# Kernel tuning notes

Measured on AMD Instinct MI355X. Metric: run time of the kernel, lower is better.

## Reference

```python
import jax, jax.numpy as jnp
import numpy as np

L, B, D_IN, H, N, NUM_LAYERS = 2048, 16, 64, 512, 64, 4


def setup_inputs() -> dict:
    key = jax.random.key(0)
    ks = jax.random.split(key, 9)
    x = jax.random.normal(ks[0], (L, B, D_IN), dtype=jnp.float32)
    enc_W = jax.random.normal(ks[1], (D_IN, H), dtype=jnp.float32) / np.sqrt(D_IN)
    enc_b = jax.random.normal(ks[2], (H,), dtype=jnp.float32) * 0.01
    # Per-layer S4D parameters, stacked along leading layer axis.
    log_dt = jax.random.uniform(ks[3], (NUM_LAYERS, H), dtype=jnp.float32,
                                minval=np.log(1e-3), maxval=np.log(1e-1))
    log_A_re = jnp.log(0.5 * jnp.ones((NUM_LAYERS, H, N), dtype=jnp.float32))
    A_im = jnp.broadcast_to(np.pi * jnp.arange(N, dtype=jnp.float32),
                            (NUM_LAYERS, H, N)).copy()
    C_re = jax.random.normal(ks[4], (NUM_LAYERS, H, N), dtype=jnp.float32)
    C_im = jax.random.normal(ks[5], (NUM_LAYERS, H, N), dtype=jnp.float32)
    Dskip = jax.random.normal(ks[6], (NUM_LAYERS, H), dtype=jnp.float32)
    return {"x": x, "enc_W": enc_W, "enc_b": enc_b, "log_dt": log_dt,
            "log_A_re": log_A_re, "A_im": A_im, "C_re": C_re, "C_im": C_im,
            "Dskip": Dskip}


def _s4d_layer(u, log_dt, log_A_re, A_im, C_re, C_im, Dskip):
    """u: [L,B,H] real. Diagonal SSM recurrent scan (ZOH discretization)."""
    dt = jnp.exp(log_dt)[:, None]                      # [H,1]
    A = -jnp.exp(log_A_re) + 1j * A_im                 # [H,N] complex, Re<0
    dA = jnp.exp(dt * A)                               # [H,N]
    dB = (dA - 1.0) / A                                # [H,N]
    C = (C_re + 1j * C_im).astype(jnp.complex64)       # [H,N]

    def step(s, u_t):                                  # s:[B,H,N] c64, u_t:[B,H]
        s = dA * s + dB * u_t[..., None]
        y = 2.0 * jnp.einsum('hn,bhn->bh', C, s).real + Dskip * u_t
        return s, y.astype(u_t.dtype)

    s0 = jnp.zeros((u.shape[1], u.shape[2], A.shape[-1]), dtype=jnp.complex64)
    sT, ys = jax.lax.scan(step, s0, u)
    return ys, sT


def reference(x, enc_W, enc_b, log_dt, log_A_re, A_im, C_re, C_im, Dskip):
    # batch_first=False: x is [L,B,D_IN]; torch code transposes to [B,L,·],
    # applies encoder, runs layers, transposes back -> equivalent to keeping
    # time-major [L,B,H] throughout.
    h = x @ enc_W + enc_b                              # [L,B,H]
    states_re, states_im = [], []
    for i in range(NUM_LAYERS):
        h, sT = _s4d_layer(h, log_dt[i], log_A_re[i], A_im[i],
                           C_re[i], C_im[i], Dskip[i])
        states_re.append(sT.real)
        states_im.append(sT.imag)
    return h, jnp.stack(states_re), jnp.stack(states_im)
```

## Files before the change

kernel.cpp:

```cpp
#include <hip/hip_runtime.h>
#include <math.h>

#define L_SEQ 2048
#define B_SZ 16
#define DIN 64
#define H_SZ 512
#define N_ST 64
#define N_LAYERS 4
#define Q_CHUNK 64
#define N_CHUNKS (L_SEQ / Q_CHUNK)
#define GSZ 4
#define N_GROUPS (N_CHUNKS / GSZ)
#define UPAD 2056
#define NTHR 768

typedef _Float16 f16;
typedef _Float16 f16x8 __attribute__((ext_vector_type(8)));
typedef _Float16 f16x4 __attribute__((ext_vector_type(4)));
typedef float    f32x4 __attribute__((ext_vector_type(4)));

struct cx { float r, i; };
__device__ __forceinline__ cx cmul(cx a, cx b) {
    return { a.r * b.r - a.i * b.i, a.r * b.i + a.i * b.r };
}

__device__ __forceinline__ void barrier_lgkm() {
    asm volatile("s_waitcnt lgkmcnt(0)\n\ts_barrier" ::: "memory");
}

__global__ __launch_bounds__(256, 4)
void encoder_mfma_kernel(const float* __restrict__ x, const float* __restrict__ W,
                         const float* __restrict__ bias, f16* __restrict__ out)
{
    __shared__ f16   x_sh[64][72];
    __shared__ f16   w_t[64][72];
    __shared__ float out_sh[64][68];
    __shared__ float b_sh[64];
    const int tid = threadIdx.x;
    const int bid = blockIdx.x;
    const int bb  = bid & 15;
    const int lt  = (bid >> 4) & 31;
    const int ht  = bid >> 9;
    const int l0 = lt * 64, h0 = ht * 64;

#pragma unroll
    for (int i = 0; i < 16; ++i) {
        int idx = tid + i * 256;
        int r = idx >> 6, c = idx & 63;
        x_sh[r][c] = (f16)x[((size_t)(l0 + r) * B_SZ + bb) * DIN + c];
        w_t[c][r]  = (f16)W[(size_t)r * H_SZ + h0 + c];
    }
    if (tid < 64) b_sh[tid] = bias[h0 + tid];
    __syncthreads();

    const int wave = tid >> 6;
    const int lane = tid & 63;
    const int frow = lane & 15;
    const int fk   = (lane >> 4) * 8;
    const int m0   = wave * 16;

    f16x8 a0 = *(const f16x8*)&w_t[m0 + frow][fk];
    f16x8 a1 = *(const f16x8*)&w_t[m0 + frow][fk + 32];
    float bv[4];
#pragma unroll
    for (int j = 0; j < 4; ++j) bv[j] = b_sh[m0 + (lane >> 4) * 4 + j];

#pragma unroll
    for (int nt = 0; nt < 4; ++nt) {
        f16x8 b0 = *(const f16x8*)&x_sh[nt * 16 + frow][fk];
        f16x8 b1 = *(const f16x8*)&x_sh[nt * 16 + frow][fk + 32];
        f32x4 acc = {0.f, 0.f, 0.f, 0.f};
        acc = __builtin_amdgcn_mfma_f32_16x16x32_f16(a0, b0, acc, 0, 0, 0);
        acc = __builtin_amdgcn_mfma_f32_16x16x32_f16(a1, b1, acc, 0, 0, 0);
#pragma unroll
        for (int j = 0; j < 4; ++j)
            out_sh[m0 + (lane >> 4) * 4 + j][nt * 16 + frow] = acc[j] + bv[j];
    }
    __syncthreads();

#pragma unroll
    for (int i = 0; i < 4; ++i) {
        int row = (tid >> 4) + i * 16;
        int c4  = (tid & 15) * 4;
        f32x4 v = *(const f32x4*)&out_sh[row][c4];
        f16x4 o;
#pragma unroll
        for (int k = 0; k < 4; ++k) o[k] = (f16)v[k];
        *(f16x4*)&out[((size_t)(h0 + row) * B_SZ + bb) * L_SEQ + l0 + c4] = o;
    }
}

__global__ __launch_bounds__(NTHR, 3)
void s4d_fused_kernel(f16* __restrict__ u_io,
                      const float* __restrict__ log_dt, const float* __restrict__ log_A_re,
                      const float* __restrict__ A_im, const float* __restrict__ C_re,
                      const float* __restrict__ C_im, const float* __restrict__ Dskip,
                      float* __restrict__ st_re, float* __restrict__ st_im)
{
    __shared__ f16   A_lds[192][72];
    __shared__ f16   G_lds[65][136];
    __shared__ f16   U_all[16][UPAD];
    __shared__ f16   S_buf[2][GSZ][16][136];
    __shared__ float dBv_sh[128];
    __shared__ float K_sh[64];
    __shared__ float w_sh[64][2];

    const int tid  = threadIdx.x;
    const int wave = tid >> 6;
    const int lane = tid & 63;
    const int h    = blockIdx.x;
    const int frow = lane & 15;
    const int fq   = lane >> 4;
    const int fk   = fq * 8;

    {
        const f16* ub = u_io + (size_t)h * B_SZ * L_SEQ;
        for (int u0 = tid; u0 < 16 * 256; u0 += NTHR) {
            int b = u0 >> 8, cidx = (u0 & 255) * 8;
            *(f16x8*)&U_all[b][cidx] = *(const f16x8*)&ub[(size_t)b * L_SEQ + cidx];
        }
    }
    f16* yb = u_io + (size_t)h * B_SZ * L_SEQ;

    for (int layer = 0; layer < N_LAYERS; ++layer) {
        const int ph = layer * H_SZ + h;
        const int pn = ph * N_ST + lane;

        {
            float dt   = expf(log_dt[ph]);
            float Are  = -expf(log_A_re[pn]);
            float Aim  = A_im[pn];
            float mg   = expf(dt * Are);
            float phs  = dt * Aim;
            cx dA1 = { mg * cosf(phs), mg * sinf(phs) };
            float invd = 1.0f / (Are * Are + Aim * Aim);
            float nr   = dA1.r - 1.0f;
            float dBr  = (nr * Are + dA1.i * Aim) * invd;
            float dBi  = (dA1.i * Are - nr * Aim) * invd;
            float Cr   = C_re[pn];
            float Ci   = C_im[pn];
            if (wave == 0) { dBv_sh[2 * lane] = dBr; dBv_sh[2 * lane + 1] = dBi; }

            const int role = wave & 3;
            const int seg  = wave >> 2;
            cx dA2  = cmul(dA1, dA1);
            cx dA4  = cmul(dA2, dA2);
            cx dA8  = cmul(dA4, dA4);
            cx dA16 = cmul(dA8, dA8);
            cx P = { 1.f, 0.f };
            int j0 = 0, jend = 21;
            if (seg >= 1) { P = cmul(cmul(dA16, dA4), dA1); j0 = 21; jend = 42; }
            if (seg == 2) { P = cmul(P, P); j0 = 42; jend = (role >= 2) ? 65 : 64; }
            for (int j = j0; j < jend; ++j) {
                if (role == 0)      A_lds[64  + lane][63 - j] = (f16)(P.r * dBr - P.i * dBi);
                else if (role == 1) A_lds[128 + lane][63 - j] = (f16)(P.r * dBi + P.i * dBr);
                else if (role == 2) G_lds[j][2 * lane]     = (f16)( 2.f * (Cr * P.r - Ci * P.i));
                else {
                    G_lds[j][2 * lane + 1] = (f16)(-2.f * (Cr * P.i + Ci * P.r));
                    if (j == 64) { w_sh[lane][0] = P.r; w_sh[lane][1] = P.i; }
                }
                P = cmul(P, dA1);
            }
        }
        barrier_lgkm();

        if (tid < 512) {
            const int t  = tid >> 3;
            const int l8 = tid & 7;
            f16x8 g0 = *(const f16x8*)&G_lds[t][l8 * 16];
            f16x8 g1 = *(const f16x8*)&G_lds[t][l8 * 16 + 8];
            f32x4 d0 = *(const f32x4*)&dBv_sh[l8 * 16];
            f32x4 d1 = *(const f32x4*)&dBv_sh[l8 * 16 + 4];
            f32x4 d2 = *(const f32x4*)&dBv_sh[l8 * 16 + 8];
            f32x4 d3 = *(const f32x4*)&dBv_sh[l8 * 16 + 12];
            float acc = 0.f;
#pragma unroll
            for (int k = 0; k < 4; ++k) {
                acc += (float)g0[k]     * d0[k];
                acc += (float)g0[k + 4] * d1[k];
                acc += (float)g1[k]     * d2[k];
                acc += (float)g1[k + 4] * d3[k];
            }
            acc += __shfl_xor(acc, 1);
            acc += __shfl_xor(acc, 2);
            acc += __shfl_xor(acc, 4);
            if (l8 == 0) K_sh[t] = acc;
        }
        barrier_lgkm();
        for (int e = tid; e < 64 * 64; e += NTHR) {
            int i = e >> 6, jc = e & 63;
            A_lds[i][jc] = (jc <= i) ? (f16)K_sh[i - jc] : (f16)0.f;
        }
        barrier_lgkm();

        const float Dv = Dskip[ph];
        f16x8 aRe0, aRe1, aIm0, aIm1;
        f16x8 aT0[2], aT1[2], aG[2][4];
        float wr4[4], wi4[4];
        float s_r[4] = {0.f,0.f,0.f,0.f}, s_i[4] = {0.f,0.f,0.f,0.f};
        if (wave < 4) {
            const int m0 = 16 * wave;
            aRe0 = *(const f16x8*)&A_lds[64  + m0 + frow][fk];
            aRe1 = *(const f16x8*)&A_lds[64  + m0 + frow][fk + 32];
            aIm0 = *(const f16x8*)&A_lds[128 + m0 + frow][fk];
            aIm1 = *(const f16x8*)&A_lds[128 + m0 + frow][fk + 32];
#pragma unroll
            for (int p = 0; p < 4; ++p) {
                int n = m0 + fq * 4 + p;
                wr4[p] = w_sh[n][0]; wi4[p] = w_sh[n][1];
            }
        } else {
            const int mh = (wave - 4) & 1;
#pragma unroll
            for (int mt = 0; mt < 2; ++mt) {
                const int r0 = 32 * mh + 16 * mt + frow;
                aT0[mt] = *(const f16x8*)&A_lds[r0][fk];
                aT1[mt] = *(const f16x8*)&A_lds[r0][fk + 32];
#pragma unroll
                for (int k4 = 0; k4 < 4; ++k4)
                    aG[mt][k4] = *(const f16x8*)&G_lds[1 + r0][fk + 32 * k4];
            }
        }
        f16x4 yh[2];

        for (int g = 0; g <= N_GROUPS + 1; ++g) {
            if (wave < 4) {
                if (g < N_GROUPS) {
                    const int gb = g & 1;
#pragma unroll
                    for (int j = 0; j < GSZ; ++j) {
                        f16x8 sf;
                        sf[0] = (f16)s_r[0]; sf[1] = (f16)s_i[0];
                        sf[2] = (f16)s_r[1]; sf[3] = (f16)s_i[1];
                        sf[4] = (f16)s_r[2]; sf[5] = (f16)s_i[2];
                        sf[6] = (f16)s_r[3]; sf[7] = (f16)s_i[3];
                        *(f16x8*)&S_buf[gb][j][frow][32 * wave + 8 * fq] = sf;
                        const int co = (g * GSZ + j) * 64;
                        f16x8 b0 = *(const f16x8*)&U_all[frow][co + fk];
                        f16x8 b1 = *(const f16x8*)&U_all[frow][co + fk + 32];
                        f32x4 aR = {0.f,0.f,0.f,0.f}, aI = {0.f,0.f,0.f,0.f};
                        aR = __builtin_amdgcn_mfma_f32_16x16x32_f16(aRe0, b0, aR, 0, 0, 0);
                        aR = __builtin_amdgcn_mfma_f32_16x16x32_f16(aRe1, b1, aR, 0, 0, 0);
                        aI = __builtin_amdgcn_mfma_f32_16x16x32_f16(aIm0, b0, aI, 0, 0, 0);
                        aI = __builtin_amdgcn_mfma_f32_16x16x32_f16(aIm1, b1, aI, 0, 0, 0);
#pragma unroll
                        for (int p = 0; p < 4; ++p) {
                            float nr2 = wr4[p] * s_r[p] - wi4[p] * s_i[p] + aR[p];
                            float ni2 = wi4[p] * s_r[p] + wr4[p] * s_i[p] + aI[p];
                            s_r[p] = nr2; s_i[p] = ni2;
                        }
                    }
                }
            } else {
                const int ow = wave - 4, jc = ow >> 1, mh = ow & 1;
                if (layer < N_LAYERS - 1 && g >= 2) {
                    const int co2 = ((g - 2) * GSZ + jc) * 64;
                    *(f16x4*)&U_all[frow][co2 + 32 * mh + fq * 4]      = yh[0];
                    *(f16x4*)&U_all[frow][co2 + 32 * mh + 16 + fq * 4] = yh[1];
                }
                if (g >= 1 && g <= N_GROUPS) {
                    const int gp = g - 1, pb = gp & 1;
                    const int co = (gp * GSZ + jc) * 64;
                    f16x8 b0 = *(const f16x8*)&U_all[frow][co + fk];
                    f16x8 b1 = *(const f16x8*)&U_all[frow][co + fk + 32];
                    f16x8 sv0 = *(const f16x8*)&S_buf[pb][jc][frow][fk];
                    f16x8 sv1 = *(const f16x8*)&S_buf[pb][jc][frow][fk + 32];
                    f16x8 sv2 = *(const f16x8*)&S_buf[pb][jc][frow][fk + 64];
                    f16x8 sv3 = *(const f16x8*)&S_buf[pb][jc][frow][fk + 96];
#pragma unroll
                    for (int mt = 0; mt < 2; ++mt) {
                        f32x4 acc = {0.f,0.f,0.f,0.f};
                        acc = __builtin_amdgcn_mfma_f32_16x16x32_f16(aT0[mt], b0, acc, 0, 0, 0);
                        acc = __builtin_amdgcn_mfma_f32_16x16x32_f16(aT1[mt], b1, acc, 0, 0, 0);
                        acc = __builtin_amdgcn_mfma_f32_16x16x32_f16(aG[mt][0], sv0, acc, 0, 0, 0);
                        acc = __builtin_amdgcn_mfma_f32_16x16x32_f16(aG[mt][1], sv1, acc, 0, 0, 0);
                        acc = __builtin_amdgcn_mfma_f32_16x16x32_f16(aG[mt][2], sv2, acc, 0, 0, 0);
                        acc = __builtin_amdgcn_mfma_f32_16x16x32_f16(aG[mt][3], sv3, acc, 0, 0, 0);
                        const int t0 = 32 * mh + 16 * mt + fq * 4;
                        f16x4 uf = *(const f16x4*)&U_all[frow][co + t0];
                        f16x4 o;
#pragma unroll
                        for (int k = 0; k < 4; ++k) o[k] = (f16)(acc[k] + Dv * (float)uf[k]);
                        if (layer == N_LAYERS - 1)
                            *(f16x4*)&yb[(size_t)frow * L_SEQ + co + t0] = o;
                        else
                            yh[mt] = o;
                    }
                }
            }
            barrier_lgkm();
        }

        if (wave < 4) {
#pragma unroll
            for (int p = 0; p < 4; ++p) {
                int n = 16 * wave + 4 * fq + p;
                size_t base = (((size_t)layer * B_SZ + frow) * H_SZ + h) * N_ST + n;
                st_re[base] = s_r[p];
                st_im[base] = s_i[p];
            }
        }
        __syncthreads();
    }
}

__global__ __launch_bounds__(256, 4)
void hbl_to_lbh_kernel(const f16* __restrict__ in, float* __restrict__ out)
{
    __shared__ float t_sh[64][65];
    const int tid = threadIdx.x, bid = blockIdx.x;
    const int bb = bid & 15, lt = (bid >> 4) & 31, ht = bid >> 9;
    const int l0 = lt * 64, h0 = ht * 64;
#pragma unroll
    for (int i = 0; i < 4; ++i) {
        int idx = tid + i * 256;
        int hh = idx >> 4, l4 = (idx & 15) * 4;
        f16x4 v = *(const f16x4*)&in[((size_t)(h0 + hh) * B_SZ + bb) * L_SEQ + l0 + l4];
#pragma unroll
        for (int k = 0; k < 4; ++k) t_sh[hh][l4 + k] = (float)v[k];
    }
    __syncthreads();
#pragma unroll
    for (int i = 0; i < 16; ++i) {
        int idx = tid + i * 256;
        int ll = idx >> 6, hh = idx & 63;
        out[((size_t)(l0 + ll) * B_SZ + bb) * H_SZ + h0 + hh] = t_sh[hh][ll];
    }
}

extern "C" void kernel_launch(void* const* d_in, const int* in_sizes, int n_in,
                              void* d_out, int out_size, void* d_ws, size_t ws_size,
                              hipStream_t stream)
{
    const float* x        = (const float*)d_in[0];
    const float* enc_W    = (const float*)d_in[1];
    const float* enc_b    = (const float*)d_in[2];
    const float* log_dt   = (const float*)d_in[3];
    const float* log_A_re = (const float*)d_in[4];
    const float* A_im     = (const float*)d_in[5];
    const float* C_re     = (const float*)d_in[6];
    const float* C_im     = (const float*)d_in[7];
    const float* Dskip    = (const float*)d_in[8];

    float* out_lbh = (float*)d_out;
    float* st_re   = out_lbh + (size_t)L_SEQ * B_SZ * H_SZ;
    float* st_im   = st_re + (size_t)N_LAYERS * B_SZ * H_SZ * N_ST;
    f16*   B0      = (f16*)d_ws;

    encoder_mfma_kernel<<<4096, 256, 0, stream>>>(x, enc_W, enc_b, B0);

    s4d_fused_kernel<<<512, NTHR, 0, stream>>>(B0, log_dt, log_A_re, A_im,
                                               C_re, C_im, Dskip, st_re, st_im);

    hbl_to_lbh_kernel<<<4096, 256, 0, stream>>>(B0, out_lbh);
}
```

Baseline: 243.3 us.

## Overlap next-layer SSM kernel setup with scan, swizzle LDS, rebalance output waves

Waves 8-11, formerly output waves, now build the next layer's A/G/K matrices during groups 1-3 of the current layer's scan. The per-layer setup with its barriers is taken off the critical path for layers 1-3. The output work is consolidated onto waves 4-7, each handling four M-tiles. U_all and S_buf padding is replaced by an XOR swizzle, and the transpose kernel now writes float4. The risk is a race: the next layer's setup overwrites A_lds/G_lds/w_sh while the current layer's waves hold register copies, which is only safe if every wave has loaded its fragments before g==1.

```diff
diff --git a/kernel.cpp b/kernel.cpp
--- a/kernel.cpp
+++ b/kernel.cpp
@@ -11,8 +11,9 @@
 #define N_CHUNKS (L_SEQ / Q_CHUNK)
 #define GSZ 4
 #define N_GROUPS (N_CHUNKS / GSZ)
-#define UPAD 2056
 #define NTHR 768
+
+#define USWZ(b, colf16) ((((colf16) * 2)) ^ (((b) & 7) << 4))
 
 typedef _Float16 f16;
 typedef _Float16 f16x8 __attribute__((ext_vector_type(8)));
@@ -99,8 +100,8 @@
 {
     __shared__ f16   A_lds[192][72];
     __shared__ f16   G_lds[65][136];
-    __shared__ f16   U_all[16][UPAD];
-    __shared__ f16   S_buf[2][GSZ][16][136];
+    __shared__ f16   U_all[16][2048];
+    __shared__ f16   S_buf[2][GSZ][16][128];
     __shared__ float dBv_sh[128];
     __shared__ float K_sh[64];
     __shared__ float w_sh[64][2];
@@ -116,8 +117,9 @@
     {
         const f16* ub = u_io + (size_t)h * B_SZ * L_SEQ;
         for (int u0 = tid; u0 < 16 * 256; u0 += NTHR) {
-            int b = u0 >> 8, cidx = (u0 & 255) * 8;
-            *(f16x8*)&U_all[b][cidx] = *(const f16x8*)&ub[(size_t)b * L_SEQ + cidx];
+            int b = u0 >> 8, c8 = (u0 & 255) * 8;
+            f16x8 v = *(const f16x8*)&ub[(size_t)b * L_SEQ + c8];
+            *(f16x8*)((char*)U_all[b] + USWZ(b, c8)) = v;
         }
     }
     f16* yb = u_io + (size_t)h * B_SZ * L_SEQ;
@@ -126,76 +128,77 @@
         const int ph = layer * H_SZ + h;
         const int pn = ph * N_ST + lane;
 
-        {
-            float dt   = expf(log_dt[ph]);
-            float Are  = -expf(log_A_re[pn]);
-            float Aim  = A_im[pn];
-            float mg   = expf(dt * Are);
-            float phs  = dt * Aim;
-            cx dA1 = { mg * cosf(phs), mg * sinf(phs) };
-            float invd = 1.0f / (Are * Are + Aim * Aim);
-            float nr   = dA1.r - 1.0f;
-            float dBr  = (nr * Are + dA1.i * Aim) * invd;
-            float dBi  = (dA1.i * Are - nr * Aim) * invd;
-            float Cr   = C_re[pn];
-            float Ci   = C_im[pn];
-            if (wave == 0) { dBv_sh[2 * lane] = dBr; dBv_sh[2 * lane + 1] = dBi; }
-
-            const int role = wave & 3;
-            const int seg  = wave >> 2;
-            cx dA2  = cmul(dA1, dA1);
-            cx dA4  = cmul(dA2, dA2);
-            cx dA8  = cmul(dA4, dA4);
-            cx dA16 = cmul(dA8, dA8);
-            cx P = { 1.f, 0.f };
-            int j0 = 0, jend = 21;
-            if (seg >= 1) { P = cmul(cmul(dA16, dA4), dA1); j0 = 21; jend = 42; }
-            if (seg == 2) { P = cmul(P, P); j0 = 42; jend = (role >= 2) ? 65 : 64; }
-            for (int j = j0; j < jend; ++j) {
-                if (role == 0)      A_lds[64  + lane][63 - j] = (f16)(P.r * dBr - P.i * dBi);
-                else if (role == 1) A_lds[128 + lane][63 - j] = (f16)(P.r * dBi + P.i * dBr);
-                else if (role == 2) G_lds[j][2 * lane]     = (f16)( 2.f * (Cr * P.r - Ci * P.i));
-                else {
-                    G_lds[j][2 * lane + 1] = (f16)(-2.f * (Cr * P.i + Ci * P.r));
-                    if (j == 64) { w_sh[lane][0] = P.r; w_sh[lane][1] = P.i; }
-                }
-                P = cmul(P, dA1);
-            }
+        if (layer == 0) {
+            {
+                float dt   = expf(log_dt[ph]);
+                float Are  = -expf(log_A_re[pn]);
+                float Aim  = A_im[pn];
+                float mg   = expf(dt * Are);
+                float phs  = dt * Aim;
+                cx dA1 = { mg * cosf(phs), mg * sinf(phs) };
+                float invd = 1.0f / (Are * Are + Aim * Aim);
+                float nr   = dA1.r - 1.0f;
+                float dBr  = (nr * Are + dA1.i * Aim) * invd;
+                float dBi  = (dA1.i * Are - nr * Aim) * invd;
+                float Cr   = C_re[pn];
+                float Ci   = C_im[pn];
+                if (wave == 0) { dBv_sh[2 * lane] = dBr; dBv_sh[2 * lane + 1] = dBi; }
+
+                const int role = wave & 3;
+                const int seg  = wave >> 2;
+                cx dA2  = cmul(dA1, dA1);
+                cx dA4  = cmul(dA2, dA2);
+                cx dA8  = cmul(dA4, dA4);
+                cx dA16 = cmul(dA8, dA8);
+                cx P = { 1.f, 0.f };
+                int j0 = 0, jend = 21;
+                if (seg >= 1) { P = cmul(cmul(dA16, dA4), dA1); j0 = 21; jend = 42; }
+                if (seg == 2) { P = cmul(P, P); j0 = 42; jend = (role >= 2) ? 65 : 64; }
+                for (int j = j0; j < jend; ++j) {
+                    if (role == 0)      A_lds[64  + lane][63 - j] = (f16)(P.r * dBr - P.i * dBi);
+                    else if (role == 1) A_lds[128 + lane][63 - j] = (f16)(P.r * dBi + P.i * dBr);
+                    else if (role == 2) G_lds[j][2 * lane]     = (f16)( 2.f * (Cr * P.r - Ci * P.i));
+                    else {
+                        G_lds[j][2 * lane + 1] = (f16)(-2.f * (Cr * P.i + Ci * P.r));
+                        if (j == 64) { w_sh[lane][0] = P.r; w_sh[lane][1] = P.i; }
+                    }
+                    P = cmul(P, dA1);
+                }
+            }
+            barrier_lgkm();
+            if (tid < 512) {
+                const int t  = tid >> 3;
+                const int l8 = tid & 7;
+                f16x8 g0 = *(const f16x8*)&G_lds[t][l8 * 16];
+                f16x8 g1 = *(const f16x8*)&G_lds[t][l8 * 16 + 8];
+                f32x4 d0 = *(const f32x4*)&dBv_sh[l8 * 16];
+                f32x4 d1 = *(const f32x4*)&dBv_sh[l8 * 16 + 4];
+                f32x4 d2 = *(const f32x4*)&dBv_sh[l8 * 16 + 8];
+                f32x4 d3 = *(const f32x4*)&dBv_sh[l8 * 16 + 12];
+                float acc = 0.f;
+#pragma unroll
+                for (int k = 0; k < 4; ++k) {
+                    acc += (float)g0[k]     * d0[k];
+                    acc += (float)g0[k + 4] * d1[k];
+                    acc += (float)g1[k]     * d2[k];
+                    acc += (float)g1[k + 4] * d3[k];
+                }
+                acc += __shfl_xor(acc, 1);
+                acc += __shfl_xor(acc, 2);
+                acc += __shfl_xor(acc, 4);
+                if (l8 == 0) K_sh[t] = acc;
+            }
+            barrier_lgkm();
+            for (int e = tid; e < 64 * 64; e += NTHR) {
+                int i = e >> 6, jc = e & 63;
+                A_lds[i][jc] = (jc <= i) ? (f16)K_sh[i - jc] : (f16)0.f;
+            }
+            barrier_lgkm();
         }
-        barrier_lgkm();
-
-        if (tid < 512) {
-            const int t  = tid >> 3;
-            const int l8 = tid & 7;
-            f16x8 g0 = *(const f16x8*)&G_lds[t][l8 * 16];
-            f16x8 g1 = *(const f16x8*)&G_lds[t][l8 * 16 + 8];
-            f32x4 d0 = *(const f32x4*)&dBv_sh[l8 * 16];
-            f32x4 d1 = *(const f32x4*)&dBv_sh[l8 * 16 + 4];
-            f32x4 d2 = *(const f32x4*)&dBv_sh[l8 * 16 + 8];
-            f32x4 d3 = *(const f32x4*)&dBv_sh[l8 * 16 + 12];
-            float acc = 0.f;
-#pragma unroll
-            for (int k = 0; k < 4; ++k) {
-                acc += (float)g0[k]     * d0[k];
-                acc += (float)g0[k + 4] * d1[k];
-                acc += (float)g1[k]     * d2[k];
-                acc += (float)g1[k + 4] * d3[k];
-            }
-            acc += __shfl_xor(acc, 1);
-            acc += __shfl_xor(acc, 2);
-            acc += __shfl_xor(acc, 4);
-            if (l8 == 0) K_sh[t] = acc;
-        }
-        barrier_lgkm();
-        for (int e = tid; e < 64 * 64; e += NTHR) {
-            int i = e >> 6, jc = e & 63;
-            A_lds[i][jc] = (jc <= i) ? (f16)K_sh[i - jc] : (f16)0.f;
-        }
-        barrier_lgkm();
 
         const float Dv = Dskip[ph];
         f16x8 aRe0, aRe1, aIm0, aIm1;
-        f16x8 aT0[2], aT1[2], aG[2][4];
+        f16x8 aT[4][2], aG[4][4];
         float wr4[4], wi4[4];
         float s_r[4] = {0.f,0.f,0.f,0.f}, s_i[4] = {0.f,0.f,0.f,0.f};
         if (wave < 4) {
@@ -209,19 +212,17 @@
                 int n = m0 + fq * 4 + p;
                 wr4[p] = w_sh[n][0]; wi4[p] = w_sh[n][1];
             }
-        } else {
-            const int mh = (wave - 4) & 1;
-#pragma unroll
-            for (int mt = 0; mt < 2; ++mt) {
-                const int r0 = 32 * mh + 16 * mt + frow;
-                aT0[mt] = *(const f16x8*)&A_lds[r0][fk];
-                aT1[mt] = *(const f16x8*)&A_lds[r0][fk + 32];
-#pragma unroll
-                for (int k4 = 0; k4 < 4; ++k4)
-                    aG[mt][k4] = *(const f16x8*)&G_lds[1 + r0][fk + 32 * k4];
+        } else if (wave < 8) {
+#pragma unroll
+            for (int mt = 0; mt < 4; ++mt) {
+                aT[mt][0] = *(const f16x8*)&A_lds[16 * mt + frow][fk];
+                aT[mt][1] = *(const f16x8*)&A_lds[16 * mt + frow][fk + 32];
+#pragma unroll
+                for (int ks = 0; ks < 4; ++ks)
+                    aG[mt][ks] = *(const f16x8*)&G_lds[1 + 16 * mt + frow][fk + 32 * ks];
             }
         }
-        f16x4 yh[2];
+        f16x4 yh[4];
 
         for (int g = 0; g <= N_GROUPS + 1; ++g) {
             if (wave < 4) {
@@ -234,10 +235,10 @@
                         sf[2] = (f16)s_r[1]; sf[3] = (f16)s_i[1];
                         sf[4] = (f16)s_r[2]; sf[5] = (f16)s_i[2];
                         sf[6] = (f16)s_r[3]; sf[7] = (f16)s_i[3];
-                        *(f16x8*)&S_buf[gb][j][frow][32 * wave + 8 * fq] = sf;
+                        *(f16x8*)((char*)S_buf[gb][j][frow] + USWZ(frow, 32 * wave + fk)) = sf;
                         const int co = (g * GSZ + j) * 64;
-                        f16x8 b0 = *(const f16x8*)&U_all[frow][co + fk];
-                        f16x8 b1 = *(const f16x8*)&U_all[frow][co + fk + 32];
+                        f16x8 b0 = *(const f16x8*)((const char*)U_all[frow] + USWZ(frow, co + fk));
+                        f16x8 b1 = *(const f16x8*)((const char*)U_all[frow] + USWZ(frow, co + fk + 32));
                         f32x4 aR = {0.f,0.f,0.f,0.f}, aI = {0.f,0.f,0.f,0.f};
                         aR = __builtin_amdgcn_mfma_f32_16x16x32_f16(aRe0, b0, aR, 0, 0, 0);
                         aR = __builtin_amdgcn_mfma_f32_16x16x32_f16(aRe1, b1, aR, 0, 0, 0);
@@ -251,33 +252,34 @@
                         }
                     }
                 }
-            } else {
-                const int ow = wave - 4, jc = ow >> 1, mh = ow & 1;
+            } else if (wave < 8) {
+                const int jc = wave - 4;
                 if (layer < N_LAYERS - 1 && g >= 2) {
                     const int co2 = ((g - 2) * GSZ + jc) * 64;
-                    *(f16x4*)&U_all[frow][co2 + 32 * mh + fq * 4]      = yh[0];
-                    *(f16x4*)&U_all[frow][co2 + 32 * mh + 16 + fq * 4] = yh[1];
+#pragma unroll
+                    for (int mt = 0; mt < 4; ++mt)
+                        *(f16x4*)((char*)U_all[frow] + USWZ(frow, co2 + 16 * mt + fq * 4)) = yh[mt];
                 }
                 if (g >= 1 && g <= N_GROUPS) {
                     const int gp = g - 1, pb = gp & 1;
                     const int co = (gp * GSZ + jc) * 64;
-                    f16x8 b0 = *(const f16x8*)&U_all[frow][co + fk];
-                    f16x8 b1 = *(const f16x8*)&U_all[frow][co + fk + 32];
-                    f16x8 sv0 = *(const f16x8*)&S_buf[pb][jc][frow][fk];
-                    f16x8 sv1 = *(const f16x8*)&S_buf[pb][jc][frow][fk + 32];
-                    f16x8 sv2 = *(const f16x8*)&S_buf[pb][jc][frow][fk + 64];
-                    f16x8 sv3 = *(const f16x8*)&S_buf[pb][jc][frow][fk + 96];
-#pragma unroll
-                    for (int mt = 0; mt < 2; ++mt) {
+                    f16x8 b0 = *(const f16x8*)((const char*)U_all[frow] + USWZ(frow, co + fk));
+                    f16x8 b1 = *(const f16x8*)((const char*)U_all[frow] + USWZ(frow, co + fk + 32));
+                    f16x8 sv0 = *(const f16x8*)((const char*)S_buf[pb][jc][frow] + USWZ(frow, fk));
+                    f16x8 sv1 = *(const f16x8*)((const char*)S_buf[pb][jc][frow] + USWZ(frow, fk + 32));
+                    f16x8 sv2 = *(const f16x8*)((const char*)S_buf[pb][jc][frow] + USWZ(frow, fk + 64));
+                    f16x8 sv3 = *(const f16x8*)((const char*)S_buf[pb][jc][frow] + USWZ(frow, fk + 96));
+#pragma unroll
+                    for (int mt = 0; mt < 4; ++mt) {
                         f32x4 acc = {0.f,0.f,0.f,0.f};
-                        acc = __builtin_amdgcn_mfma_f32_16x16x32_f16(aT0[mt], b0, acc, 0, 0, 0);
-                        acc = __builtin_amdgcn_mfma_f32_16x16x32_f16(aT1[mt], b1, acc, 0, 0, 0);
+                        acc = __builtin_amdgcn_mfma_f32_16x16x32_f16(aT[mt][0], b0, acc, 0, 0, 0);
+                        acc = __builtin_amdgcn_mfma_f32_16x16x32_f16(aT[mt][1], b1, acc, 0, 0, 0);
                         acc = __builtin_amdgcn_mfma_f32_16x16x32_f16(aG[mt][0], sv0, acc, 0, 0, 0);
                         acc = __builtin_amdgcn_mfma_f32_16x16x32_f16(aG[mt][1], sv1, acc, 0, 0, 0);
                         acc = __builtin_amdgcn_mfma_f32_16x16x32_f16(aG[mt][2], sv2, acc, 0, 0, 0);
                         acc = __builtin_amdgcn_mfma_f32_16x16x32_f16(aG[mt][3], sv3, acc, 0, 0, 0);
-                        const int t0 = 32 * mh + 16 * mt + fq * 4;
-                        f16x4 uf = *(const f16x4*)&U_all[frow][co + t0];
+                        const int t0 = 16 * mt + fq * 4;
+                        f16x4 uf = *(const f16x4*)((const char*)U_all[frow] + USWZ(frow, co + t0));
                         f16x4 o;
 #pragma unroll
                         for (int k = 0; k < 4; ++k) o[k] = (f16)(acc[k] + Dv * (float)uf[k]);
@@ -285,6 +287,76 @@
                             *(f16x4*)&yb[(size_t)frow * L_SEQ + co + t0] = o;
                         else
                             yh[mt] = o;
+                    }
+                }
+            } else {
+                if (layer < N_LAYERS - 1) {
+                    if (g == 1) {
+                        const int ph2 = (layer + 1) * H_SZ + h;
+                        const int pn2 = ph2 * N_ST + lane;
+                        float dt   = expf(log_dt[ph2]);
+                        float Are  = -expf(log_A_re[pn2]);
+                        float Aim  = A_im[pn2];
+                        float mg   = expf(dt * Are);
+                        float phs  = dt * Aim;
+                        cx dA1 = { mg * cosf(phs), mg * sinf(phs) };
+                        float invd = 1.0f / (Are * Are + Aim * Aim);
+                        float nr   = dA1.r - 1.0f;
+                        float dBr  = (nr * Are + dA1.i * Aim) * invd;
+                        float dBi  = (dA1.i * Are - nr * Aim) * invd;
+                        float Cr   = C_re[pn2];
+                        float Ci   = C_im[pn2];
+                        if (wave == 8) { dBv_sh[2 * lane] = dBr; dBv_sh[2 * lane + 1] = dBi; }
+                        cx dA2  = cmul(dA1, dA1);
+                        cx dA4  = cmul(dA2, dA2);
+                        cx dA8  = cmul(dA4, dA4);
+                        cx dA16 = cmul(dA8, dA8);
+                        cx dA32 = cmul(dA16, dA16);
+                        if (wave == 8 || wave == 9) {
+                            cx P = { 1.f, 0.f };
+                            int j0 = 0, jend = 32;
+                            if (wave == 9) { P = dA32; j0 = 32; jend = 64; }
+                            for (int j = j0; j < jend; ++j) {
+                                A_lds[64  + lane][63 - j] = (f16)(P.r * dBr - P.i * dBi);
+                                A_lds[128 + lane][63 - j] = (f16)(P.r * dBi + P.i * dBr);
+                                P = cmul(P, dA1);
+                            }
+                        } else {
+                            cx P = { 1.f, 0.f };
+                            int j0 = 0, jend = 33;
+                            if (wave == 11) { P = cmul(dA32, dA1); j0 = 33; jend = 65; }
+                            for (int j = j0; j < jend; ++j) {
+                                G_lds[j][2 * lane]     = (f16)( 2.f * (Cr * P.r - Ci * P.i));
+                                G_lds[j][2 * lane + 1] = (f16)(-2.f * (Cr * P.i + Ci * P.r));
+                                if (j == 64) { w_sh[lane][0] = P.r; w_sh[lane][1] = P.i; }
+                                P = cmul(P, dA1);
+                            }
+                        }
+                    } else if (g == 2) {
+                        const int idx = tid - 512;
+                        const int t   = idx >> 2;
+                        const int l4  = idx & 3;
+                        const int base = l4 * 32;
+                        f16x8 g0 = *(const f16x8*)&G_lds[t][base];
+                        f16x8 g1 = *(const f16x8*)&G_lds[t][base + 8];
+                        f16x8 g2 = *(const f16x8*)&G_lds[t][base + 16];
+                        f16x8 g3 = *(const f16x8*)&G_lds[t][base + 24];
+                        float acc = 0.f;
+#pragma unroll
+                        for (int k = 0; k < 8; ++k) {
+                            acc += (float)g0[k] * dBv_sh[base + k];
+                            acc += (float)g1[k] * dBv_sh[base + 8 + k];
+                            acc += (float)g2[k] * dBv_sh[base + 16 + k];
+                            acc += (float)g3[k] * dBv_sh[base + 24 + k];
+                        }
+                        acc += __shfl_xor(acc, 1);
+                        acc += __shfl_xor(acc, 2);
+                        if (l4 == 0) K_sh[t] = acc;
+                    } else if (g == 3) {
+                        for (int e = tid - 512; e < 64 * 64; e += 256) {
+                            int i = e >> 6, jc2 = e & 63;
+                            A_lds[i][jc2] = (jc2 <= i) ? (f16)K_sh[i - jc2] : (f16)0.f;
+                        }
                     }
                 }
             }
@@ -321,10 +393,12 @@
     }
     __syncthreads();
 #pragma unroll
-    for (int i = 0; i < 16; ++i) {
+    for (int i = 0; i < 4; ++i) {
         int idx = tid + i * 256;
-        int ll = idx >> 6, hh = idx & 63;
-        out[((size_t)(l0 + ll) * B_SZ + bb) * H_SZ + h0 + hh] = t_sh[hh][ll];
+        int ll = idx >> 4, h4 = (idx & 15) * 4;
+        float4 o = make_float4(t_sh[h4][ll], t_sh[h4 + 1][ll],
+                               t_sh[h4 + 2][ll], t_sh[h4 + 3][ll]);
+        *(float4*)&out[((size_t)(l0 + ll) * B_SZ + bb) * H_SZ + h0 + h4] = o;
     }
 }
 
```

Measured after the change: 352.9 us. 45.1% more time.
